# Performance work log

Measured on AMD Instinct MI355X. Metric: run time of the kernel, lower is better.

## Reference

```python
import jax, jax.numpy as jnp
import numpy as np

N_FILTERS = 8
FILTER_LEN = 31
PAD = (FILTER_LEN - 1) // 2  # 15
B, L = 64, 131072


def setup_inputs() -> dict:
    key = jax.random.key(0)
    ks = jax.random.split(key, 7)
    x = jax.random.normal(ks[0], (B, L), dtype=jnp.float32)
    features = jax.random.normal(ks[1], (B, N_FILTERS), dtype=jnp.float32)
    # learned params
    filter_params = jax.random.normal(ks[2], (N_FILTERS, 1, FILTER_LEN), dtype=jnp.float32)
    # selector MLP (torch Linear convention: W is (out, in))
    lim = 1.0 / np.sqrt(N_FILTERS)
    W1 = jax.random.uniform(ks[3], (N_FILTERS, N_FILTERS), minval=-lim, maxval=lim, dtype=jnp.float32)
    b1 = jax.random.uniform(ks[4], (N_FILTERS,), minval=-lim, maxval=lim, dtype=jnp.float32)
    W2 = jax.random.uniform(ks[5], (N_FILTERS, N_FILTERS), minval=-lim, maxval=lim, dtype=jnp.float32)
    b2 = jax.random.uniform(ks[6], (N_FILTERS,), minval=-lim, maxval=lim, dtype=jnp.float32)
    return {"x": x, "features": features, "filter_params": filter_params,
            "W1": W1, "b1": b1, "W2": W2, "b2": b2}


def reference(x, features, filter_params, W1, b1, W2, b2):
    # conv1d (cross-correlation, as in torch): (B,1,L) * (F,1,K) -> (B,F,L)
    xp = x[:, None, :]
    filtered = jax.lax.conv_general_dilated(
        xp, filter_params,
        window_strides=(1,), padding=[(PAD, PAD)],
        dimension_numbers=('NCH', 'OIH', 'NCH'))
    # per-sample soft filter selection
    h = jax.nn.relu(features @ W1.T + b1)
    weights = jax.nn.softmax(h @ W2.T + b2, axis=-1)  # (B, F)
    # weighted sum over filter channels -> (B, L)
    out = jnp.einsum('bfl,bf->bl', filtered, weights)
    return out
```

## Files before the change

kernel.cpp:

```cpp
#include <hip/hip_runtime.h>
#include <math.h>

#define BB 64
#define LL 131072
#define NF 8
#define FLEN 31

#define TPB 256
#define RPT 8
#define TILE (TPB * RPT)
#define TCELLS (TILE / 4)
#define NCELLS (TCELLS + 8)
#define ROWCELLS (LL / 4)

typedef float f32x4 __attribute__((ext_vector_type(4)));

#define SWZ(c) ((c) ^ (((c) >> 3) & 7))

__global__ __launch_bounds__(TPB, 6) void adaptive_filter_fused(
    const float* __restrict__ x,
    const float* __restrict__ features,
    const float* __restrict__ fp,
    const float* __restrict__ W1,
    const float* __restrict__ b1,
    const float* __restrict__ W2,
    const float* __restrict__ b2,
    float* __restrict__ out)
{
    const int tiles_per_row = LL / TILE;
    const int row  = blockIdx.x / tiles_per_row;
    const int tile = blockIdx.x % tiles_per_row;
    const int tid  = threadIdx.x;

    __shared__ f32x4 lds4[NCELLS];
    __shared__ float cs[32];

    const f32x4* xrow4 = reinterpret_cast<const f32x4*>(x + (size_t)row * LL);
    const int cell_base = tile * TCELLS - 4;

    const int d0 = tid, d1 = tid + TPB, d2 = tid + 2 * TPB;
    const unsigned gc0 = (unsigned)(cell_base + d0);
    const unsigned gc1 = (unsigned)(cell_base + d1);
    const unsigned gc2 = (unsigned)(cell_base + d2);
    f32x4 v0 = (f32x4)(0.0f);
    f32x4 v1 = v0, v2 = v0;
    if (gc0 < ROWCELLS) v0 = xrow4[gc0];
    if (gc1 < ROWCELLS) v1 = xrow4[gc1];
    const bool has2 = (tid < NCELLS - 2 * TPB);
    if (has2 && gc2 < ROWCELLS) v2 = xrow4[gc2];

    if (tid < FLEN) {
        const int t = tid;
        float f[NF];
        #pragma unroll
        for (int j = 0; j < NF; ++j) f[j] = features[row * NF + j];

        float h[NF];
        #pragma unroll
        for (int i = 0; i < NF; ++i) {
            float s = b1[i];
            #pragma unroll
            for (int j = 0; j < NF; ++j) s = fmaf(f[j], W1[i * NF + j], s);
            h[i] = fmaxf(s, 0.0f);
        }

        float w[NF];
        float m = -1e30f;
        #pragma unroll
        for (int i = 0; i < NF; ++i) {
            float s = b2[i];
            #pragma unroll
            for (int j = 0; j < NF; ++j) s = fmaf(h[j], W2[i * NF + j], s);
            w[i] = s;
            m = fmaxf(m, s);
        }
        float denom = 0.0f;
        #pragma unroll
        for (int i = 0; i < NF; ++i) { w[i] = expf(w[i] - m); denom += w[i]; }
        const float inv = 1.0f / denom;

        float s = 0.0f;
        #pragma unroll
        for (int ff = 0; ff < NF; ++ff) s = fmaf(w[ff] * inv, fp[ff * FLEN + t], s);
        cs[t] = s;
    }

    lds4[SWZ(d0)] = v0;
    lds4[SWZ(d1)] = v1;
    if (has2) lds4[SWZ(d2)] = v2;

    __syncthreads();

    const float tv = cs[tid & 31];
    float tap[FLEN];
    #pragma unroll
    for (int t = 0; t < FLEN; ++t)
        tap[t] = __int_as_float(__builtin_amdgcn_readlane(__float_as_int(tv), t));

    float wA[20], wB[20];
    #pragma unroll
    for (int k = 0; k < 5; ++k) {
        const f32x4 v = lds4[SWZ(2 * tid + k)];
        wA[4 * k + 0] = v.x; wA[4 * k + 1] = v.y;
        wA[4 * k + 2] = v.z; wA[4 * k + 3] = v.w;
    }
    #pragma unroll
    for (int k = 0; k < 5; ++k) {
        const f32x4 v = lds4[SWZ(2 * tid + 5 + k)];
        wB[4 * k + 0] = v.x; wB[4 * k + 1] = v.y;
        wB[4 * k + 2] = v.z; wB[4 * k + 3] = v.w;
    }

    float acc[RPT];
    #pragma unroll
    for (int r = 0; r < RPT; ++r) acc[r] = 0.0f;

    #pragma unroll
    for (int r = 0; r < RPT; ++r) {
        #pragma unroll
        for (int t = 0; t <= 18 - r; ++t)
            acc[r] = fmaf(tap[t], wA[r + 1 + t], acc[r]);
        #pragma unroll
        for (int t = 19 - r; t < FLEN; ++t)
            acc[r] = fmaf(tap[t], wB[r + t - 19], acc[r]);
    }

    f32x4* orow4 = reinterpret_cast<f32x4*>(out + (size_t)row * LL) + tile * TCELLS;
    f32x4 s0; s0.x = acc[0]; s0.y = acc[1]; s0.z = acc[2]; s0.w = acc[3];
    f32x4 s1; s1.x = acc[4]; s1.y = acc[5]; s1.z = acc[6]; s1.w = acc[7];
    __builtin_nontemporal_store(s0, &orow4[2 * tid + 0]);
    __builtin_nontemporal_store(s1, &orow4[2 * tid + 1]);
}

extern "C" void kernel_launch(void* const* d_in, const int* in_sizes, int n_in,
                              void* d_out, int out_size, void* d_ws, size_t ws_size,
                              hipStream_t stream) {
    const float* x        = (const float*)d_in[0];
    const float* features = (const float*)d_in[1];
    const float* fp       = (const float*)d_in[2];
    const float* W1       = (const float*)d_in[3];
    const float* b1       = (const float*)d_in[4];
    const float* W2       = (const float*)d_in[5];
    const float* b2       = (const float*)d_in[6];
    float* out = (float*)d_out;

    const int grid = BB * (LL / TILE);
    adaptive_filter_fused<<<grid, TPB, 0, stream>>>(x, features, fp, W1, b1, W2, b2, out);
}
```

Measured before the change: 19.95 us.

## Process four tiles per block with double-buffered LDS and prefetch

Result: faster. 19.18 us (-3.8%).

```diff
diff --git a/kernel.cpp b/kernel.cpp
--- a/kernel.cpp
+++ b/kernel.cpp
@@ -11,13 +11,22 @@
 #define TILE (TPB * RPT)
 #define TCELLS (TILE / 4)
 #define NCELLS (TCELLS + 8)
+#define NTILE 4
+#define GRPS (LL / TILE / NTILE)
 #define ROWCELLS (LL / 4)
 
 typedef float f32x4 __attribute__((ext_vector_type(4)));
 
 #define SWZ(c) ((c) ^ (((c) >> 3) & 7))
 
-__global__ __launch_bounds__(TPB, 6) void adaptive_filter_fused(
+#define LIGHT_BARRIER() do {                                  \
+    __builtin_amdgcn_sched_barrier(0);                        \
+    asm volatile("s_waitcnt lgkmcnt(0)" ::: "memory");        \
+    __builtin_amdgcn_s_barrier();                             \
+    __builtin_amdgcn_sched_barrier(0);                        \
+} while (0)
+
+__global__ __launch_bounds__(TPB, 4) void adaptive_filter_fused(
     const float* __restrict__ x,
     const float* __restrict__ features,
     const float* __restrict__ fp,
@@ -27,27 +36,29 @@
     const float* __restrict__ b2,
     float* __restrict__ out)
 {
-    const int tiles_per_row = LL / TILE;
-    const int row  = blockIdx.x / tiles_per_row;
-    const int tile = blockIdx.x % tiles_per_row;
-    const int tid  = threadIdx.x;
+    const int row = blockIdx.x / GRPS;
+    const int grp = blockIdx.x % GRPS;
+    const int tid = threadIdx.x;
 
-    __shared__ f32x4 lds4[NCELLS];
+    __shared__ f32x4 lds4[2][NCELLS];
     __shared__ float cs[32];
 
     const f32x4* xrow4 = reinterpret_cast<const f32x4*>(x + (size_t)row * LL);
-    const int cell_base = tile * TCELLS - 4;
+    f32x4* orowbase4 = reinterpret_cast<f32x4*>(out + (size_t)row * LL);
 
     const int d0 = tid, d1 = tid + TPB, d2 = tid + 2 * TPB;
-    const unsigned gc0 = (unsigned)(cell_base + d0);
-    const unsigned gc1 = (unsigned)(cell_base + d1);
-    const unsigned gc2 = (unsigned)(cell_base + d2);
-    f32x4 v0 = (f32x4)(0.0f);
-    f32x4 v1 = v0, v2 = v0;
-    if (gc0 < ROWCELLS) v0 = xrow4[gc0];
-    if (gc1 < ROWCELLS) v1 = xrow4[gc1];
     const bool has2 = (tid < NCELLS - 2 * TPB);
-    if (has2 && gc2 < ROWCELLS) v2 = xrow4[gc2];
+
+    f32x4 pv0 = (f32x4)(0.0f), pv1 = pv0, pv2 = pv0;
+    {
+        const int cb = (grp * NTILE) * TCELLS - 4;
+        const unsigned g0 = (unsigned)(cb + d0);
+        const unsigned g1 = (unsigned)(cb + d1);
+        const unsigned g2 = (unsigned)(cb + d2);
+        if (g0 < ROWCELLS) pv0 = __builtin_nontemporal_load(&xrow4[g0]);
+        if (g1 < ROWCELLS) pv1 = __builtin_nontemporal_load(&xrow4[g1]);
+        if (has2 && g2 < ROWCELLS) pv2 = __builtin_nontemporal_load(&xrow4[g2]);
+    }
 
     if (tid < FLEN) {
         const int t = tid;
@@ -85,51 +96,72 @@
         cs[t] = s;
     }
 
-    lds4[SWZ(d0)] = v0;
-    lds4[SWZ(d1)] = v1;
-    if (has2) lds4[SWZ(d2)] = v2;
-
-    __syncthreads();
-
-    const float tv = cs[tid & 31];
     float tap[FLEN];
-    #pragma unroll
-    for (int t = 0; t < FLEN; ++t)
-        tap[t] = __int_as_float(__builtin_amdgcn_readlane(__float_as_int(tv), t));
-
-    float wA[20], wB[20];
-    #pragma unroll
-    for (int k = 0; k < 5; ++k) {
-        const f32x4 v = lds4[SWZ(2 * tid + k)];
-        wA[4 * k + 0] = v.x; wA[4 * k + 1] = v.y;
-        wA[4 * k + 2] = v.z; wA[4 * k + 3] = v.w;
-    }
-    #pragma unroll
-    for (int k = 0; k < 5; ++k) {
-        const f32x4 v = lds4[SWZ(2 * tid + 5 + k)];
-        wB[4 * k + 0] = v.x; wB[4 * k + 1] = v.y;
-        wB[4 * k + 2] = v.z; wB[4 * k + 3] = v.w;
-    }
-
-    float acc[RPT];
-    #pragma unroll
-    for (int r = 0; r < RPT; ++r) acc[r] = 0.0f;
 
     #pragma unroll
-    for (int r = 0; r < RPT; ++r) {
+    for (int k = 0; k < NTILE; ++k) {
+        const int buf = k & 1;
+        const int tile = grp * NTILE + k;
+
+        lds4[buf][SWZ(d0)] = pv0;
+        lds4[buf][SWZ(d1)] = pv1;
+        if (has2) lds4[buf][SWZ(d2)] = pv2;
+
+        if (k + 1 < NTILE) {
+            const int cb = (tile + 1) * TCELLS - 4;
+            const unsigned g0 = (unsigned)(cb + d0);
+            const unsigned g1 = (unsigned)(cb + d1);
+            const unsigned g2 = (unsigned)(cb + d2);
+            f32x4 n0 = (f32x4)(0.0f), n1 = n0, n2 = n0;
+            if (g0 < ROWCELLS) n0 = __builtin_nontemporal_load(&xrow4[g0]);
+            if (g1 < ROWCELLS) n1 = __builtin_nontemporal_load(&xrow4[g1]);
+            if (has2 && g2 < ROWCELLS) n2 = __builtin_nontemporal_load(&xrow4[g2]);
+            pv0 = n0; pv1 = n1; pv2 = n2;
+        }
+
+        LIGHT_BARRIER();
+
+        if (k == 0) {
+            const float tv = cs[tid & 31];
+            #pragma unroll
+            for (int t = 0; t < FLEN; ++t)
+                tap[t] = __int_as_float(__builtin_amdgcn_readlane(__float_as_int(tv), t));
+        }
+
+        float wA[20], wB[20];
         #pragma unroll
-        for (int t = 0; t <= 18 - r; ++t)
-            acc[r] = fmaf(tap[t], wA[r + 1 + t], acc[r]);
+        for (int q = 0; q < 5; ++q) {
+            const f32x4 v = lds4[buf][SWZ(2 * tid + q)];
+            wA[4 * q + 0] = v.x; wA[4 * q + 1] = v.y;
+            wA[4 * q + 2] = v.z; wA[4 * q + 3] = v.w;
+        }
         #pragma unroll
-        for (int t = 19 - r; t < FLEN; ++t)
-            acc[r] = fmaf(tap[t], wB[r + t - 19], acc[r]);
+        for (int q = 0; q < 5; ++q) {
+            const f32x4 v = lds4[buf][SWZ(2 * tid + 5 + q)];
+            wB[4 * q + 0] = v.x; wB[4 * q + 1] = v.y;
+            wB[4 * q + 2] = v.z; wB[4 * q + 3] = v.w;
+        }
+
+        float acc[RPT];
+        #pragma unroll
+        for (int r = 0; r < RPT; ++r) acc[r] = 0.0f;
+
+        #pragma unroll
+        for (int r = 0; r < RPT; ++r) {
+            #pragma unroll
+            for (int t = 0; t <= 18 - r; ++t)
+                acc[r] = fmaf(tap[t], wA[r + 1 + t], acc[r]);
+            #pragma unroll
+            for (int t = 19 - r; t < FLEN; ++t)
+                acc[r] = fmaf(tap[t], wB[r + t - 19], acc[r]);
+        }
+
+        f32x4* orow4 = orowbase4 + tile * TCELLS;
+        f32x4 s0; s0.x = acc[0]; s0.y = acc[1]; s0.z = acc[2]; s0.w = acc[3];
+        f32x4 s1; s1.x = acc[4]; s1.y = acc[5]; s1.z = acc[6]; s1.w = acc[7];
+        __builtin_nontemporal_store(s0, &orow4[2 * tid + 0]);
+        __builtin_nontemporal_store(s1, &orow4[2 * tid + 1]);
     }
-
-    f32x4* orow4 = reinterpret_cast<f32x4*>(out + (size_t)row * LL) + tile * TCELLS;
-    f32x4 s0; s0.x = acc[0]; s0.y = acc[1]; s0.z = acc[2]; s0.w = acc[3];
-    f32x4 s1; s1.x = acc[4]; s1.y = acc[5]; s1.z = acc[6]; s1.w = acc[7];
-    __builtin_nontemporal_store(s0, &orow4[2 * tid + 0]);
-    __builtin_nontemporal_store(s1, &orow4[2 * tid + 1]);
 }
 
 extern "C" void kernel_launch(void* const* d_in, const int* in_sizes, int n_in,
@@ -144,6 +176,6 @@
     const float* b2       = (const float*)d_in[6];
     float* out = (float*)d_out;
 
-    const int grid = BB * (LL / TILE);
+    const int grid = BB * GRPS;
     adaptive_filter_fused<<<grid, TPB, 0, stream>>>(x, features, fp, W1, b1, W2, b2, out);
 }
```
